# Kernel tuning notes

Hardware: AMD Instinct MI355X
Metric: run time of the kernel (lower is better)

The kernel has to match this reference:

```python
import jax, jax.numpy as jnp
import numpy as np

B, C, H, W = 4, 256, 64, 64


def conv1x1(x, w, b):
    # x: [B,C,H,W], w: [O,C] (1x1 kernel squeezed), b: [O]
    return jnp.einsum('bchw,oc->bohw', x, w) + b[None, :, None, None]


def setup_inputs() -> dict:
    key = jax.random.key(0)
    ks = jax.random.split(key, 7)
    fuse = jax.random.normal(ks[0], (B, C, H, W), dtype=jnp.float32)
    scale = 0.02
    Wq = jax.random.normal(ks[1], (C, C), dtype=jnp.float32) * scale
    bq = jnp.zeros((C,), dtype=jnp.float32)
    Wk = jax.random.normal(ks[2], (C, C), dtype=jnp.float32) * scale
    bk = jnp.zeros((C,), dtype=jnp.float32)
    Wv = jax.random.normal(ks[3], (C, C), dtype=jnp.float32) * scale
    bv = jnp.zeros((C,), dtype=jnp.float32)
    return {'fuse': fuse, 'Wq': Wq, 'bq': bq, 'Wk': Wk, 'bk': bk, 'Wv': Wv, 'bv': bv}


def reference(fuse, Wq, bq, Wk, bk, Wv, bv):
    b, c, h, w = fuse.shape
    hw = h * w
    scale = 1.0 / (c ** 0.5)
    Q = conv1x1(fuse, Wq, bq).reshape(b, c, hw)          # [B, C, HW]
    K = conv1x1(fuse, Wk, bk).reshape(b, c, hw)          # [B, C, HW]
    # Q_mask: reshape [B,C,HW] -> [B*H, C*W], max over rows -> [1, C*W]
    Q_mask = jnp.max(Q.reshape(b * h, c * w), axis=0, keepdims=True)
    # scores: [B, HW(query), HW(key)]
    scores = jnp.einsum('bcn,bcm->bnm', Q, K) * scale
    # NOTE: softmax over dim=0 (batch axis), faithful to the torch source
    soft = jax.nn.softmax(scores, axis=0)
    m = jnp.max(soft, axis=1)                             # [B, HW]
    m = jnp.max(m.reshape(-1, w), axis=-1, keepdims=True) # [B*H, 1]
    mask = (m @ Q_mask).reshape(b, c, h, w)               # [B*H,1]x[1,C*W]
    V = conv1x1(fuse, Wv, bv)
    return V + V * mask
```

## Files before the change

kernel.cpp:

```cpp
#include <hip/hip_runtime.h>
#include <stdint.h>

#define HW 4096
#define CH 256
#define NB 4

typedef __attribute__((ext_vector_type(8))) short bf16x8;
typedef __attribute__((ext_vector_type(4))) float f32x4;
typedef __attribute__((ext_vector_type(2))) long longx2;
typedef unsigned char u8;

__device__ __forceinline__ ushort f2bf(float f) {
    uint32_t u = __float_as_uint(f);
    u += 0x7fffu + ((u >> 16) & 1u);
    return (ushort)(u >> 16);
}
__device__ __forceinline__ uint fkey(float f) {
    uint b = __float_as_uint(f);
    return ((int)b < 0) ? ~b : (b | 0x80000000u);
}
__device__ __forceinline__ float finv(uint k) {
    uint b = (k & 0x80000000u) ? (k ^ 0x80000000u) : ~k;
    return __uint_as_float(b);
}

__device__ __forceinline__ size_t fragidx(int b, int o, int hw) {
    return ((((size_t)b * 8 + (o >> 5)) * 128 + (hw >> 5)) * 1024)
         + ((((o >> 3) & 3) * 16 + (hw & 15)) * 16)
         + (((hw >> 4) & 1) * 8) + (o & 7);
}

__global__ __launch_bounds__(256) void prep_kernel(
    const float* __restrict__ Wq, const float* __restrict__ Wk,
    const float* __restrict__ Wv,
    ushort* __restrict__ Wq16, ushort* __restrict__ Wk16,
    ushort* __restrict__ Wv16, unsigned int* __restrict__ m2k,
    unsigned int* __restrict__ qmk) {
    int i = blockIdx.x * 256 + threadIdx.x;
    Wq16[i] = f2bf(Wq[i]);
    Wk16[i] = f2bf(Wk[i]);
    Wv16[i] = f2bf(Wv[i]);
    if (i < NB * HW) qmk[i] = 0;
    if (i < NB * 64) m2k[i] = 0;
}

__global__ __launch_bounds__(256) void convQK_kernel(
    const float* __restrict__ fuse,
    const ushort* __restrict__ Wq16, const ushort* __restrict__ Wk16,
    const float* __restrict__ bq, const float* __restrict__ bk,
    u8* __restrict__ Qw8, u8* __restrict__ Kw8,
    unsigned int* __restrict__ qmout) {
    __shared__ __align__(16) ushort WqLs[256][72];
    __shared__ __align__(16) ushort WkLs[256][72];
    __shared__ __align__(16) float tileF[64][65];
    __shared__ __align__(16) ushort Bls[64][72];
    __shared__ float qred[4][4][64];
    const int t = threadIdx.x;
    const int lane = t & 63, w = t >> 6;
    const int hw0 = blockIdx.x * 64;
    const int b = blockIdx.y;
    f32x4 accQ[4][4] = {}, accK[4][4] = {};
    for (int kc = 0; kc < 4; ++kc) {
        __syncthreads();
        #pragma unroll
        for (int i = 0; i < 8; ++i) {
            int q = t + 256 * i;
            int row = q >> 3, c8 = (q & 7) * 8;
            *(int4*)&WqLs[row][c8] =
                *(const int4*)(Wq16 + (size_t)row * CH + kc * 64 + c8);
            *(int4*)&WkLs[row][c8] =
                *(const int4*)(Wk16 + (size_t)row * CH + kc * 64 + c8);
        }
        {
            const int c = t >> 2, q4 = (t & 3) * 16;
            const float* src = fuse + ((size_t)b * CH + kc * 64 + c) * HW + hw0 + q4;
            #pragma unroll
            for (int q = 0; q < 4; ++q) {
                float4 v = *(const float4*)(src + q * 4);
                tileF[c][q4 + q * 4 + 0] = v.x; tileF[c][q4 + q * 4 + 1] = v.y;
                tileF[c][q4 + q * 4 + 2] = v.z; tileF[c][q4 + q * 4 + 3] = v.w;
            }
        }
        __syncthreads();
        #pragma unroll
        for (int rep = 0; rep < 2; ++rep) {
            int u = t + rep * 256;
            int hw = u >> 3, i8 = (u & 7) * 8;
            __align__(16) ushort o8[8];
            #pragma unroll
            for (int k = 0; k < 8; ++k) o8[k] = f2bf(tileF[i8 + k][hw]);
            *(int4*)&Bls[hw][i8] = *(const int4*)o8;
        }
        __syncthreads();
        #pragma unroll
        for (int kk = 0; kk < 2; ++kk) {
            bf16x8 aq[4], ak[4];
            #pragma unroll
            for (int rf = 0; rf < 4; ++rf) {
                aq[rf] = *(const bf16x8*)&WqLs[w * 64 + rf * 16 + (lane & 15)]
                                              [kk * 32 + (lane >> 4) * 8];
                ak[rf] = *(const bf16x8*)&WkLs[w * 64 + rf * 16 + (lane & 15)]
                                              [kk * 32 + (lane >> 4) * 8];
            }
            #pragma unroll
            for (int cf = 0; cf < 4; ++cf) {
                bf16x8 bf_ = *(const bf16x8*)&Bls[cf * 16 + (lane & 15)]
                                                 [kk * 32 + (lane >> 4) * 8];
                #pragma unroll
                for (int rf = 0; rf < 4; ++rf) {
                    accQ[rf][cf] = __builtin_amdgcn_mfma_f32_16x16x32_bf16(
                        aq[rf], bf_, accQ[rf][cf], 0, 0, 0);
                    accK[rf][cf] = __builtin_amdgcn_mfma_f32_16x16x32_bf16(
                        ak[rf], bf_, accK[rf][cf], 0, 0, 0);
                }
            }
        }
    }
    float qmx[4][4];
    #pragma unroll
    for (int cf = 0; cf < 4; ++cf)
        #pragma unroll
        for (int r = 0; r < 4; ++r) qmx[cf][r] = -3.4e38f;
    #pragma unroll
    for (int rf = 0; rf < 4; ++rf) {
        const int ob = w * 64 + rf * 16 + (lane >> 4) * 4;
        #pragma unroll
        for (int cf = 0; cf < 4; ++cf) {
            const int hw = hw0 + cf * 16 + (lane & 15);
            size_t idx = fragidx(b, ob, hw);
            {
                float v0 = accQ[rf][cf][0] + bq[ob + 0];
                float v1 = accQ[rf][cf][1] + bq[ob + 1];
                float v2 = accQ[rf][cf][2] + bq[ob + 2];
                float v3 = accQ[rf][cf][3] + bq[ob + 3];
                int u = __builtin_amdgcn_cvt_pk_fp8_f32(v0, v1, 0, false);
                u = __builtin_amdgcn_cvt_pk_fp8_f32(v2, v3, u, true);
                *(unsigned int*)&Qw8[idx] = (unsigned int)u;
                qmx[cf][0] = fmaxf(qmx[cf][0], v0);
                qmx[cf][1] = fmaxf(qmx[cf][1], v1);
                qmx[cf][2] = fmaxf(qmx[cf][2], v2);
                qmx[cf][3] = fmaxf(qmx[cf][3], v3);
            }
            {
                float v0 = accK[rf][cf][0] + bk[ob + 0];
                float v1 = accK[rf][cf][1] + bk[ob + 1];
                float v2 = accK[rf][cf][2] + bk[ob + 2];
                float v3 = accK[rf][cf][3] + bk[ob + 3];
                int u = __builtin_amdgcn_cvt_pk_fp8_f32(v0, v1, 0, false);
                u = __builtin_amdgcn_cvt_pk_fp8_f32(v2, v3, u, true);
                *(unsigned int*)&Kw8[idx] = (unsigned int)u;
            }
        }
    }
    #pragma unroll
    for (int cf = 0; cf < 4; ++cf)
        #pragma unroll
        for (int r = 0; r < 4; ++r) {
            float v = qmx[cf][r];
            v = fmaxf(v, __shfl_xor(v, 16));
            v = fmaxf(v, __shfl_xor(v, 32));
            qmx[cf][r] = v;
        }
    __syncthreads();
    if (lane < 16) {
        #pragma unroll
        for (int cf = 0; cf < 4; ++cf)
            #pragma unroll
            for (int r = 0; r < 4; ++r)
                qred[w][r][cf * 16 + lane] = qmx[cf][r];
    }
    __syncthreads();
    {
        const int r = t >> 6, h64 = t & 63;
        float v = fmaxf(fmaxf(qred[0][r][h64], qred[1][r][h64]),
                        fmaxf(qred[2][r][h64], qred[3][r][h64]));
        atomicMax(qmout + r * HW + hw0 + h64, fkey(v));
    }
}

__global__ __launch_bounds__(256) void convV_kernel(
    const float* __restrict__ fuse, const ushort* __restrict__ Wv16,
    const float* __restrict__ bv, float* __restrict__ outf,
    const unsigned int* __restrict__ m2key,
    const unsigned int* __restrict__ qmkey) {
    __shared__ __align__(16) ushort Als[256][72];
    __shared__ __align__(16) float tileF[64][65];
    __shared__ __align__(16) ushort Bls[64][72];
    __shared__ float m2s[64];
    const int t = threadIdx.x;
    const int lane = t & 63, w = t >> 6;
    const int hw0 = blockIdx.x * 64;
    const int b = blockIdx.y;
    if (t < 64) m2s[t] = __uint_as_float(m2key[b * 64 + t]);
    f32x4 acc[4][4] = {};
    for (int kc = 0; kc < 4; ++kc) {
        __syncthreads();
        #pragma unroll
        for (int i = 0; i < 8; ++i) {
            int q = t + 256 * i;
            int row = q >> 3, c8 = (q & 7) * 8;
            *(int4*)&Als[row][c8] =
                *(const int4*)(Wv16 + (size_t)row * CH + kc * 64 + c8);
        }
        {
            const int c = t >> 2, q4 = (t & 3) * 16;
            const float* src = fuse + ((size_t)b * CH + kc * 64 + c) * HW + hw0 + q4;
            #pragma unroll
            for (int q = 0; q < 4; ++q) {
                float4 v = *(const float4*)(src + q * 4);
                tileF[c][q4 + q * 4 + 0] = v.x; tileF[c][q4 + q * 4 + 1] = v.y;
                tileF[c][q4 + q * 4 + 2] = v.z; tileF[c][q4 + q * 4 + 3] = v.w;
            }
        }
        __syncthreads();
        #pragma unroll
        for (int rep = 0; rep < 2; ++rep) {
            int u = t + rep * 256;
            int hw = u >> 3, i8 = (u & 7) * 8;
            __align__(16) ushort o8[8];
            #pragma unroll
            for (int k = 0; k < 8; ++k) o8[k] = f2bf(tileF[i8 + k][hw]);
            *(int4*)&Bls[hw][i8] = *(const int4*)o8;
        }
        __syncthreads();
        #pragma unroll
        for (int kk = 0; kk < 2; ++kk) {
            bf16x8 af[4];
            #pragma unroll
            for (int rf = 0; rf < 4; ++rf)
                af[rf] = *(const bf16x8*)&Als[w * 64 + rf * 16 + (lane & 15)]
                                             [kk * 32 + (lane >> 4) * 8];
            #pragma unroll
            for (int cf = 0; cf < 4; ++cf) {
                bf16x8 bf_ = *(const bf16x8*)&Bls[cf * 16 + (lane & 15)]
                                                 [kk * 32 + (lane >> 4) * 8];
                #pragma unroll
                for (int rf = 0; rf < 4; ++rf)
                    acc[rf][cf] = __builtin_amdgcn_mfma_f32_16x16x32_bf16(
                        af[rf], bf_, acc[rf][cf], 0, 0, 0);
            }
        }
    }
    #pragma unroll
    for (int rf = 0; rf < 4; ++rf) {
        const int ob = w * 64 + rf * 16 + (lane >> 4) * 4;
        #pragma unroll
        for (int cf = 0; cf < 4; ++cf) {
            const int hw = hw0 + cf * 16 + (lane & 15);
            const float mv = m2s[ob >> 2];
            #pragma unroll
            for (int r = 0; r < 4; ++r) {
                float vv = acc[rf][cf][r] + bv[ob + r];
                float qm = finv(qmkey[r * HW + hw]);
                outf[((size_t)b * CH + ob + r) * HW + hw] = vv * (1.0f + mv * qm);
            }
        }
    }
}

__global__ __launch_bounds__(256, 2) void scores64(
    const u8* __restrict__ Qw, const u8* __restrict__ Kw,
    unsigned int* __restrict__ m2k) {
    __shared__ __align__(16) f32x4 EX[4][4][4][64];
    __shared__ float red[4][4];
    const int t = threadIdx.x;
    const int lane = t & 63, w = t >> 6;
    const int bid = blockIdx.x;
    const int xcd = bid & 7, j = bid >> 3;
    const int vm = xcd * 8 + (j & 7);
    const int s  = j >> 3;

    const u8* kp = Kw + (((size_t)w * 8) * 128 + vm * 2) * 1024 + lane * 16;
    const u8* qp0 = Qw + (((size_t)w * 8) * 128 + (s * 8) * 2) * 1024 + lane * 16;

    longx2 BK[8][2];
    #pragma unroll
    for (int kc = 0; kc < 8; ++kc)
        #pragma unroll
        for (int p = 0; p < 2; ++p)
            BK[kc][p] = *(const longx2*)(kp + (size_t)kc * 131072 + p * 1024);

    longx2 AQ[8][2];
#define LOADQ(IT)                                                          \
    _Pragma("unroll") for (int kc = 0; kc < 8; ++kc)                       \
        _Pragma("unroll") for (int p = 0; p < 2; ++p)                      \
            AQ[kc][p] = *(const longx2*)(qp0 + (IT) * 2048                 \
                                         + (size_t)kc * 131072 + p * 1024);
    LOADQ(0)

    float pmAll[4] = {0.f, 0.f, 0.f, 0.f};
    #pragma unroll
    for (int it = 0; it < 8; ++it) {
        f32x4 acc[4][4] = {};
        #pragma unroll
        for (int kc = 0; kc < 8; ++kc) {
            #pragma unroll
            for (int mf = 0; mf < 4; ++mf) {
                long bf_ = BK[kc][mf >> 1][mf & 1];
                #pragma unroll
                for (int nf = 0; nf < 4; ++nf)
                    acc[nf][mf] = __builtin_amdgcn_mfma_f32_16x16x32_fp8_fp8(
                        AQ[kc][nf >> 1][nf & 1], bf_, acc[nf][mf], 0, 0, 0);
            }
        }
        if (it + 1 < 8) { LOADQ(it + 1) }

        if (it) __syncthreads();
        #pragma unroll
        for (int nf = 0; nf < 4; ++nf)
            #pragma unroll
            for (int mf = 0; mf < 4; ++mf)
                EX[w][nf][mf][lane] = acc[nf][mf];
        __syncthreads();
        #pragma unroll
        for (int nf = 0; nf < 4; ++nf) {
            f32x4 sv[4];
            #pragma unroll
            for (int b2 = 0; b2 < 4; ++b2)
                sv[b2] = EX[b2][nf][w][lane];
            #pragma unroll
            for (int jj = 0; jj < 4; ++jj) {
                float e0 = __expf(sv[0][jj] * 0.0625f);
                float e1 = __expf(sv[1][jj] * 0.0625f);
                float e2 = __expf(sv[2][jj] * 0.0625f);
                float e3 = __expf(sv[3][jj] * 0.0625f);
                float inv = __fdividef(1.0f, e0 + e1 + e2 + e3);
                pmAll[0] = fmaxf(pmAll[0], e0 * inv);
                pmAll[1] = fmaxf(pmAll[1], e1 * inv);
                pmAll[2] = fmaxf(pmAll[2], e2 * inv);
                pmAll[3] = fmaxf(pmAll[3], e3 * inv);
            }
        }
    }
#undef LOADQ
    #pragma unroll
    for (int off = 32; off >= 1; off >>= 1) {
        pmAll[0] = fmaxf(pmAll[0], __shfl_xor(pmAll[0], off));
        pmAll[1] = fmaxf(pmAll[1], __shfl_xor(pmAll[1], off));
        pmAll[2] = fmaxf(pmAll[2], __shfl_xor(pmAll[2], off));
        pmAll[3] = fmaxf(pmAll[3], __shfl_xor(pmAll[3], off));
    }
    __syncthreads();
    if (lane == 0) {
        #pragma unroll
        for (int b2 = 0; b2 < 4; ++b2) red[w][b2] = pmAll[b2];
    }
    __syncthreads();
    if (t < 4) {
        float v = fmaxf(fmaxf(red[0][t], red[1][t]),
                        fmaxf(red[2][t], red[3][t]));
        atomicMax(m2k + t * 64 + vm, __float_as_uint(v));
    }
}

extern "C" void kernel_launch(void* const* d_in, const int* in_sizes, int n_in,
                              void* d_out, int out_size, void* d_ws, size_t ws_size,
                              hipStream_t stream) {
    const float* fuse = (const float*)d_in[0];
    const float* Wq   = (const float*)d_in[1];
    const float* bq   = (const float*)d_in[2];
    const float* Wk   = (const float*)d_in[3];
    const float* bk   = (const float*)d_in[4];
    const float* Wv   = (const float*)d_in[5];
    const float* bv   = (const float*)d_in[6];
    float* out = (float*)d_out;

    char* ws = (char*)d_ws;
    ushort* Wq16  = (ushort*)(ws);
    ushort* Wk16  = (ushort*)(ws + 131072);
    ushort* Wv16  = (ushort*)(ws + 262144);
    u8*     Qw8   = (u8*)    (ws + 393216);
    u8*     Kw8   = (u8*)    (ws + 4587520);
    unsigned int* QMK = (unsigned int*)(ws + 8781824);
    unsigned int* M2K = (unsigned int*)(ws + 8847360);

    prep_kernel<<<256, 256, 0, stream>>>(Wq, Wk, Wv, Wq16, Wk16, Wv16, M2K, QMK);
    convQK_kernel<<<dim3(64, NB), 256, 0, stream>>>(
        fuse, Wq16, Wk16, bq, bk, Qw8, Kw8, QMK);
    scores64<<<512, 256, 0, stream>>>(Qw8, Kw8, M2K);
    convV_kernel<<<dim3(64, NB), 256, 0, stream>>>(
        fuse, Wv16, bv, out, M2K, QMK);
}
```

Before: 72.03 us.

## Pack weights in MFMA fragment order, read from global, halve conv tiles

Weights are reordered during prep into MFMA A-fragment order, so the conv kernels load A operands directly from global/L2 rather than staging the full 256x64 weight slices in LDS. This cuts LDS use to a small pooled buffer, and the HW tile is halved to 32 to double the grid to 128x4 blocks with launch_bounds(256,2), raising occupancy. The scores kernel swaps __syncthreads for a custom lgkmcnt-only wait plus barrier, and pins the fp8 operand registers with empty asm to control scheduling. The risks are repeated global weight reads per block and fewer MFMAs per block to amortise overhead.

```diff
diff --git a/kernel.cpp b/kernel.cpp
--- a/kernel.cpp
+++ b/kernel.cpp
@@ -23,11 +23,23 @@
     uint b = (k & 0x80000000u) ? (k ^ 0x80000000u) : ~k;
     return __uint_as_float(b);
 }
+__device__ __forceinline__ void keepl(longx2& v) { asm volatile("" : "+v"(v)); }
+
+#define LGK_BAR()                                                        \
+    do {                                                                 \
+        asm volatile("s_waitcnt lgkmcnt(0)" ::: "memory");               \
+        __builtin_amdgcn_sched_barrier(0);                               \
+        asm volatile("s_barrier" ::: "memory");                          \
+    } while (0)
 
 __device__ __forceinline__ size_t fragidx(int b, int o, int hw) {
     return ((((size_t)b * 8 + (o >> 5)) * 128 + (hw >> 5)) * 1024)
          + ((((o >> 3) & 3) * 16 + (hw & 15)) * 16)
          + (((hw >> 4) & 1) * 8) + (o & 7);
+}
+__device__ __forceinline__ int wpackidx(int o, int c) {
+    return (((c >> 5) * 16 + (o >> 4)) * 64 + ((c >> 3) & 3) * 16 + (o & 15)) * 8
+         + (c & 7);
 }
 
 __global__ __launch_bounds__(256) void prep_kernel(
@@ -37,55 +49,45 @@
     ushort* __restrict__ Wv16, unsigned int* __restrict__ m2k,
     unsigned int* __restrict__ qmk) {
     int i = blockIdx.x * 256 + threadIdx.x;
-    Wq16[i] = f2bf(Wq[i]);
-    Wk16[i] = f2bf(Wk[i]);
-    Wv16[i] = f2bf(Wv[i]);
+    int o = i >> 8, c = i & 255;
+    int idx = wpackidx(o, c);
+    Wq16[idx] = f2bf(Wq[i]);
+    Wk16[idx] = f2bf(Wk[i]);
+    Wv16[idx] = f2bf(Wv[i]);
     if (i < NB * HW) qmk[i] = 0;
     if (i < NB * 64) m2k[i] = 0;
 }
 
-__global__ __launch_bounds__(256) void convQK_kernel(
+__global__ __launch_bounds__(256, 2) void convQK_kernel(
     const float* __restrict__ fuse,
     const ushort* __restrict__ Wq16, const ushort* __restrict__ Wk16,
     const float* __restrict__ bq, const float* __restrict__ bk,
     u8* __restrict__ Qw8, u8* __restrict__ Kw8,
     unsigned int* __restrict__ qmout) {
-    __shared__ __align__(16) ushort WqLs[256][72];
-    __shared__ __align__(16) ushort WkLs[256][72];
-    __shared__ __align__(16) float tileF[64][65];
-    __shared__ __align__(16) ushort Bls[64][72];
-    __shared__ float qred[4][4][64];
+    __shared__ __align__(16) char cpool[13056];
+    float (*tileF)[33]   = (float(*)[33])cpool;
+    ushort (*Bls)[72]    = (ushort(*)[72])(cpool + 8448);
+    float (*qred)[4][32] = (float(*)[4][32])cpool;
     const int t = threadIdx.x;
     const int lane = t & 63, w = t >> 6;
-    const int hw0 = blockIdx.x * 64;
+    const int hw0 = blockIdx.x * 32;
     const int b = blockIdx.y;
-    f32x4 accQ[4][4] = {}, accK[4][4] = {};
+    f32x4 accQ[4][2] = {}, accK[4][2] = {};
     for (int kc = 0; kc < 4; ++kc) {
         __syncthreads();
-        #pragma unroll
-        for (int i = 0; i < 8; ++i) {
-            int q = t + 256 * i;
-            int row = q >> 3, c8 = (q & 7) * 8;
-            *(int4*)&WqLs[row][c8] =
-                *(const int4*)(Wq16 + (size_t)row * CH + kc * 64 + c8);
-            *(int4*)&WkLs[row][c8] =
-                *(const int4*)(Wk16 + (size_t)row * CH + kc * 64 + c8);
-        }
         {
-            const int c = t >> 2, q4 = (t & 3) * 16;
-            const float* src = fuse + ((size_t)b * CH + kc * 64 + c) * HW + hw0 + q4;
-            #pragma unroll
-            for (int q = 0; q < 4; ++q) {
+            const int c = t >> 2, h8 = (t & 3) * 8;
+            const float* src = fuse + ((size_t)b * CH + kc * 64 + c) * HW + hw0 + h8;
+            #pragma unroll
+            for (int q = 0; q < 2; ++q) {
                 float4 v = *(const float4*)(src + q * 4);
-                tileF[c][q4 + q * 4 + 0] = v.x; tileF[c][q4 + q * 4 + 1] = v.y;
-                tileF[c][q4 + q * 4 + 2] = v.z; tileF[c][q4 + q * 4 + 3] = v.w;
-            }
-        }
-        __syncthreads();
-        #pragma unroll
-        for (int rep = 0; rep < 2; ++rep) {
-            int u = t + rep * 256;
-            int hw = u >> 3, i8 = (u & 7) * 8;
+                tileF[c][h8 + q * 4 + 0] = v.x; tileF[c][h8 + q * 4 + 1] = v.y;
+                tileF[c][h8 + q * 4 + 2] = v.z; tileF[c][h8 + q * 4 + 3] = v.w;
+            }
+        }
+        __syncthreads();
+        {
+            const int hw = t >> 3, i8 = (t & 7) * 8;
             __align__(16) ushort o8[8];
             #pragma unroll
             for (int k = 0; k < 8; ++k) o8[k] = f2bf(tileF[i8 + k][hw]);
@@ -95,15 +97,14 @@
         #pragma unroll
         for (int kk = 0; kk < 2; ++kk) {
             bf16x8 aq[4], ak[4];
+            const int fb = ((kc * 2 + kk) * 16 + w * 4) * 512 + lane * 8;
             #pragma unroll
             for (int rf = 0; rf < 4; ++rf) {
-                aq[rf] = *(const bf16x8*)&WqLs[w * 64 + rf * 16 + (lane & 15)]
-                                              [kk * 32 + (lane >> 4) * 8];
-                ak[rf] = *(const bf16x8*)&WkLs[w * 64 + rf * 16 + (lane & 15)]
-                                              [kk * 32 + (lane >> 4) * 8];
-            }
-            #pragma unroll
-            for (int cf = 0; cf < 4; ++cf) {
+                aq[rf] = *(const bf16x8*)(Wq16 + fb + rf * 512);
+                ak[rf] = *(const bf16x8*)(Wk16 + fb + rf * 512);
+            }
+            #pragma unroll
+            for (int cf = 0; cf < 2; ++cf) {
                 bf16x8 bf_ = *(const bf16x8*)&Bls[cf * 16 + (lane & 15)]
                                                  [kk * 32 + (lane >> 4) * 8];
                 #pragma unroll
@@ -116,16 +117,16 @@
             }
         }
     }
-    float qmx[4][4];
-    #pragma unroll
-    for (int cf = 0; cf < 4; ++cf)
+    float qmx[2][4];
+    #pragma unroll
+    for (int cf = 0; cf < 2; ++cf)
         #pragma unroll
         for (int r = 0; r < 4; ++r) qmx[cf][r] = -3.4e38f;
     #pragma unroll
     for (int rf = 0; rf < 4; ++rf) {
         const int ob = w * 64 + rf * 16 + (lane >> 4) * 4;
         #pragma unroll
-        for (int cf = 0; cf < 4; ++cf) {
+        for (int cf = 0; cf < 2; ++cf) {
             const int hw = hw0 + cf * 16 + (lane & 15);
             size_t idx = fragidx(b, ob, hw);
             {
@@ -153,7 +154,7 @@
         }
     }
     #pragma unroll
-    for (int cf = 0; cf < 4; ++cf)
+    for (int cf = 0; cf < 2; ++cf)
         #pragma unroll
         for (int r = 0; r < 4; ++r) {
             float v = qmx[cf][r];
@@ -164,59 +165,50 @@
     __syncthreads();
     if (lane < 16) {
         #pragma unroll
-        for (int cf = 0; cf < 4; ++cf)
+        for (int cf = 0; cf < 2; ++cf)
             #pragma unroll
             for (int r = 0; r < 4; ++r)
                 qred[w][r][cf * 16 + lane] = qmx[cf][r];
     }
     __syncthreads();
-    {
-        const int r = t >> 6, h64 = t & 63;
-        float v = fmaxf(fmaxf(qred[0][r][h64], qred[1][r][h64]),
-                        fmaxf(qred[2][r][h64], qred[3][r][h64]));
-        atomicMax(qmout + r * HW + hw0 + h64, fkey(v));
-    }
-}
-
-__global__ __launch_bounds__(256) void convV_kernel(
+    if (t < 128) {
+        const int r = t >> 5, h = t & 31;
+        float v = fmaxf(fmaxf(qred[0][r][h], qred[1][r][h]),
+                        fmaxf(qred[2][r][h], qred[3][r][h]));
+        atomicMax(qmout + r * HW + hw0 + h, fkey(v));
+    }
+}
+
+__global__ __launch_bounds__(256, 2) void convV_kernel(
     const float* __restrict__ fuse, const ushort* __restrict__ Wv16,
     const float* __restrict__ bv, float* __restrict__ outf,
     const unsigned int* __restrict__ m2key,
     const unsigned int* __restrict__ qmkey) {
-    __shared__ __align__(16) ushort Als[256][72];
-    __shared__ __align__(16) float tileF[64][65];
-    __shared__ __align__(16) ushort Bls[64][72];
+    __shared__ __align__(16) char cpool[13056];
+    float (*tileF)[33] = (float(*)[33])cpool;
+    ushort (*Bls)[72]  = (ushort(*)[72])(cpool + 8448);
     __shared__ float m2s[64];
     const int t = threadIdx.x;
     const int lane = t & 63, w = t >> 6;
-    const int hw0 = blockIdx.x * 64;
+    const int hw0 = blockIdx.x * 32;
     const int b = blockIdx.y;
     if (t < 64) m2s[t] = __uint_as_float(m2key[b * 64 + t]);
-    f32x4 acc[4][4] = {};
+    f32x4 acc[4][2] = {};
     for (int kc = 0; kc < 4; ++kc) {
         __syncthreads();
-        #pragma unroll
-        for (int i = 0; i < 8; ++i) {
-            int q = t + 256 * i;
-            int row = q >> 3, c8 = (q & 7) * 8;
-            *(int4*)&Als[row][c8] =
-                *(const int4*)(Wv16 + (size_t)row * CH + kc * 64 + c8);
-        }
         {
-            const int c = t >> 2, q4 = (t & 3) * 16;
-            const float* src = fuse + ((size_t)b * CH + kc * 64 + c) * HW + hw0 + q4;
-            #pragma unroll
-            for (int q = 0; q < 4; ++q) {
+            const int c = t >> 2, h8 = (t & 3) * 8;
+            const float* src = fuse + ((size_t)b * CH + kc * 64 + c) * HW + hw0 + h8;
+            #pragma unroll
+            for (int q = 0; q < 2; ++q) {
                 float4 v = *(const float4*)(src + q * 4);
-                tileF[c][q4 + q * 4 + 0] = v.x; tileF[c][q4 + q * 4 + 1] = v.y;
-                tileF[c][q4 + q * 4 + 2] = v.z; tileF[c][q4 + q * 4 + 3] = v.w;
-            }
-        }
-        __syncthreads();
-        #pragma unroll
-        for (int rep = 0; rep < 2; ++rep) {
-            int u = t + rep * 256;
-            int hw = u >> 3, i8 = (u & 7) * 8;
+                tileF[c][h8 + q * 4 + 0] = v.x; tileF[c][h8 + q * 4 + 1] = v.y;
+                tileF[c][h8 + q * 4 + 2] = v.z; tileF[c][h8 + q * 4 + 3] = v.w;
+            }
+        }
+        __syncthreads();
+        {
+            const int hw = t >> 3, i8 = (t & 7) * 8;
             __align__(16) ushort o8[8];
             #pragma unroll
             for (int k = 0; k < 8; ++k) o8[k] = f2bf(tileF[i8 + k][hw]);
@@ -226,12 +218,12 @@
         #pragma unroll
         for (int kk = 0; kk < 2; ++kk) {
             bf16x8 af[4];
+            const int fb = ((kc * 2 + kk) * 16 + w * 4) * 512 + lane * 8;
             #pragma unroll
             for (int rf = 0; rf < 4; ++rf)
-                af[rf] = *(const bf16x8*)&Als[w * 64 + rf * 16 + (lane & 15)]
-                                             [kk * 32 + (lane >> 4) * 8];
-            #pragma unroll
-            for (int cf = 0; cf < 4; ++cf) {
+                af[rf] = *(const bf16x8*)(Wv16 + fb + rf * 512);
+            #pragma unroll
+            for (int cf = 0; cf < 2; ++cf) {
                 bf16x8 bf_ = *(const bf16x8*)&Bls[cf * 16 + (lane & 15)]
                                                  [kk * 32 + (lane >> 4) * 8];
                 #pragma unroll
@@ -245,7 +237,7 @@
     for (int rf = 0; rf < 4; ++rf) {
         const int ob = w * 64 + rf * 16 + (lane >> 4) * 4;
         #pragma unroll
-        for (int cf = 0; cf < 4; ++cf) {
+        for (int cf = 0; cf < 2; ++cf) {
             const int hw = hw0 + cf * 16 + (lane & 15);
             const float mv = m2s[ob >> 2];
             #pragma unroll
@@ -270,7 +262,7 @@
     const int vm = xcd * 8 + (j & 7);
     const int s  = j >> 3;
 
-    const u8* kp = Kw + (((size_t)w * 8) * 128 + vm * 2) * 1024 + lane * 16;
+    const u8* kp  = Kw + (((size_t)w * 8) * 128 + vm * 2) * 1024 + lane * 16;
     const u8* qp0 = Qw + (((size_t)w * 8) * 128 + (s * 8) * 2) * 1024 + lane * 16;
 
     longx2 BK[8][2];
@@ -279,6 +271,10 @@
         #pragma unroll
         for (int p = 0; p < 2; ++p)
             BK[kc][p] = *(const longx2*)(kp + (size_t)kc * 131072 + p * 1024);
+    #pragma unroll
+    for (int kc = 0; kc < 8; ++kc)
+        #pragma unroll
+        for (int p = 0; p < 2; ++p) keepl(BK[kc][p]);
 
     longx2 AQ[8][2];
 #define LOADQ(IT)                                                          \
@@ -286,11 +282,15 @@
         _Pragma("unroll") for (int p = 0; p < 2; ++p)                      \
             AQ[kc][p] = *(const longx2*)(qp0 + (IT) * 2048                 \
                                          + (size_t)kc * 131072 + p * 1024);
+#define KEEPQ()                                                            \
+    _Pragma("unroll") for (int kc = 0; kc < 8; ++kc)                       \
+        _Pragma("unroll") for (int p = 0; p < 2; ++p) keepl(AQ[kc][p]);
     LOADQ(0)
 
     float pmAll[4] = {0.f, 0.f, 0.f, 0.f};
     #pragma unroll
     for (int it = 0; it < 8; ++it) {
+        KEEPQ()
         f32x4 acc[4][4] = {};
         #pragma unroll
         for (int kc = 0; kc < 8; ++kc) {
@@ -305,13 +305,13 @@
         }
         if (it + 1 < 8) { LOADQ(it + 1) }
 
-        if (it) __syncthreads();
+        if (it) LGK_BAR();
         #pragma unroll
         for (int nf = 0; nf < 4; ++nf)
             #pragma unroll
             for (int mf = 0; mf < 4; ++mf)
                 EX[w][nf][mf][lane] = acc[nf][mf];
-        __syncthreads();
+        LGK_BAR();
         #pragma unroll
         for (int nf = 0; nf < 4; ++nf) {
             f32x4 sv[4];
@@ -333,6 +333,7 @@
         }
     }
 #undef LOADQ
+#undef KEEPQ
     #pragma unroll
     for (int off = 32; off >= 1; off >>= 1) {
         pmAll[0] = fmaxf(pmAll[0], __shfl_xor(pmAll[0], off));
@@ -375,9 +376,9 @@
     unsigned int* M2K = (unsigned int*)(ws + 8847360);
 
     prep_kernel<<<256, 256, 0, stream>>>(Wq, Wk, Wv, Wq16, Wk16, Wv16, M2K, QMK);
-    convQK_kernel<<<dim3(64, NB), 256, 0, stream>>>(
+    convQK_kernel<<<dim3(128, NB), 256, 0, stream>>>(
         fuse, Wq16, Wk16, bq, bk, Qw8, Kw8, QMK);
     scores64<<<512, 256, 0, stream>>>(Qw8, Kw8, M2K);
-    convV_kernel<<<dim3(64, NB), 256, 0, stream>>>(
+    convV_kernel<<<dim3(128, NB), 256, 0, stream>>>(
         fuse, Wv16, bv, out, M2K, QMK);
 }
```

Result: faster. 65.91 us (-8.5%).
